# Kernel optimization log

Measured on AMD Instinct MI355X. Metric: run time of the kernel, lower is better.

The kernel has to match this reference:

```python
import jax, jax.numpy as jnp
import numpy as np

N = 100000       # nodes
E = 1600000      # undirected edges (one direction stored)
D = 64           # feature_dim


def _linear_params(key, fan_in, fan_out):
    kw, kb = jax.random.split(key)
    s = 1.0 / np.sqrt(fan_in)
    W = jax.random.uniform(kw, (fan_in, fan_out), jnp.float32, -s, s)
    b = jax.random.uniform(kb, (fan_out,), jnp.float32, -s, s)
    return W, b


def setup_inputs() -> dict:
    key = jax.random.key(0)
    ks = jax.random.split(key, 8)
    node_features = jax.random.normal(ks[0], (N, D), jnp.float32)
    node_operations = jax.random.normal(ks[1], (N, 4), jnp.float32)

    # Unique undirected edges, no self-loops -> torch's set() dedup of
    # {outgoing} U {incoming} neighbors equals counting each stored edge once
    # in both directions.
    rng = np.random.default_rng(0)
    src = rng.integers(0, N, size=4 * E)
    dst = rng.integers(0, N, size=4 * E)
    lo, hi = np.minimum(src, dst), np.maximum(src, dst)
    keep = lo != hi
    pairs = np.unique(np.stack([lo[keep], hi[keep]], axis=1), axis=0)
    assert pairs.shape[0] >= E
    perm = rng.permutation(pairs.shape[0])[:E]
    edge_index = jnp.asarray(pairs[perm].T, dtype=jnp.int32)  # [2, E]

    # node_generator: Linear(2D,128)-ReLU-Linear(128,64)-ReLU-Linear(64,D+3)
    W1, b1 = _linear_params(ks[2], 2 * D, 128)
    W2, b2 = _linear_params(ks[3], 128, 64)
    W3, b3 = _linear_params(ks[4], 64, D + 3)
    # insertion_predictor: Linear(D,32)-ReLU-Linear(32,1)-Sigmoid
    P1, pb1 = _linear_params(ks[5], D, 32)
    P2, pb2 = _linear_params(ks[6], 32, 1)

    return {
        'node_features': node_features,
        'node_operations': node_operations,
        'edge_index': edge_index,
        'W1': W1, 'b1': b1, 'W2': W2, 'b2': b2, 'W3': W3, 'b3': b3,
        'P1': P1, 'pb1': pb1, 'P2': P2, 'pb2': pb2,
    }


def reference(node_features, node_operations, edge_index,
              W1, b1, W2, b2, W3, b3, P1, pb1, P2, pb2):
    n = node_features.shape[0]
    src, dst = edge_index[0], edge_index[1]

    # candidate mask: softmax over op logits, class 0 = insert, threshold 0.5
    insert_probs = jax.nn.softmax(node_operations, axis=-1)[:, 0]
    ones = jnp.ones(src.shape[0], node_features.dtype)
    deg = (jax.ops.segment_sum(ones, src, num_segments=n)
           + jax.ops.segment_sum(ones, dst, num_segments=n))
    # torch loop skips candidates with no neighbors
    mask = (insert_probs > 0.5) & (deg > 0)
    maskf = mask.astype(node_features.dtype)

    # batched neighbor mean (undirected: both edge directions)
    nsum = (jax.ops.segment_sum(node_features[dst], src, num_segments=n)
            + jax.ops.segment_sum(node_features[src], dst, num_segments=n))
    nmean = nsum / jnp.maximum(deg, 1.0)[:, None]

    ctx = jnp.concatenate([node_features, nmean], axis=-1)  # [N, 2D]
    h = jax.nn.relu(ctx @ W1 + b1)
    h = jax.nn.relu(h @ W2 + b2)
    gen = h @ W3 + b3                         # [N, D+3]
    pos = gen[:, :3]                          # [N, 3]
    feats = gen[:, 3:]                        # [N, D]
    p = jax.nn.relu(feats @ P1 + pb1)
    prob = jax.nn.sigmoid(p @ P2 + pb2)       # [N, 1]

    # pack: [positions | features | probability], zeroed for non-candidates
    out = jnp.concatenate([pos, feats, prob], axis=-1) * maskf[:, None]
    return out
```

## Files before the change

### kernel.cpp

```cpp
#include <hip/hip_runtime.h>
#include <hip/hip_bf16.h>
#include <hip/hip_fp16.h>
#include <math.h>

typedef unsigned int u32;
typedef unsigned short u16;
typedef unsigned long long u64;

#define O_W1 0
#define O_b1 16384
#define O_W2 16512
#define O_b2 24704
#define O_W3 24768
#define O_b3 29056
#define O_P1 29123
#define O_pb1 31171
#define O_P2 31203
#define O_pb2 31235
#define W_TOTAL 31236

#define NPB 16
#define LDW 17

__device__ __forceinline__ float ldf(const void* p, long i, int dt) {
  if (dt == 1) { u32 v = ((const u16*)p)[i]; return __uint_as_float(v << 16); }
  if (dt == 2) { __half h = ((const __half*)p)[i]; return __half2float(h); }
  return ((const float*)p)[i];
}
__device__ __forceinline__ int ldei(const int* p, long i, int is64) {
  return is64 ? p[2 * i] : p[i];
}
__device__ __forceinline__ int bit_test(const u64* bits, int i) {
  return (int)((bits[i >> 6] >> (i & 63)) & 1ull);
}

extern "C" __global__ void kall_detect(const u32* __restrict__ feat,
                                       const u32* __restrict__ w1,
                                       const u32* __restrict__ ops,
                                       const u32* __restrict__ ei,
                                       int* __restrict__ hdr)
{
  int lane = threadIdx.x;
  int mode = blockIdx.x;
  if (mode == 3) {
    unsigned long long m0 = __ballot(ei[lane] == 0u);
    unsigned long long m1 = __ballot(ei[64 + lane] == 0u);
    if (lane == 0) hdr[2] = (__popcll(m0) + __popcll(m1) >= 32) ? 1 : 0;
    return;
  }
  const u32* p = (mode == 0) ? feat : (mode == 1) ? w1 : ops;
  int slot = (mode == 0) ? 0 : (mode == 1) ? 1 : 3;
  u32 w0 = p[lane];
  u32 w1v = p[64 + lane];
  u16 h[4] = { (u16)(w0 & 0xffff), (u16)(w0 >> 16),
               (u16)(w1v & 0xffff), (u16)(w1v >> 16) };
  int cb = 0;
#pragma unroll
  for (int t = 0; t < 4; ++t) {
    int e8 = (h[t] >> 7) & 0xff;
    cb += (e8 >= 110 && e8 <= 140) ? 1 : 0;
  }
  int ch = 0;
#pragma unroll
  for (int t = 0; t < 4; t += 2) {
    int e5 = (h[t] >> 10) & 0x1f;
    ch += (e5 >= 5 && e5 <= 18) ? 1 : 0;
  }
  __shared__ int sb[64], sh[64];
  sb[lane] = cb; sh[lane] = ch;
  __syncthreads();
  if (lane == 0) {
    int CB = 0, CH = 0;
    for (int t = 0; t < 64; ++t) { CB += sb[t]; CH += sh[t]; }
    int dt;
    if (CB >= 200) dt = 1;
    else if (CH >= 100) dt = 2;
    else dt = 0;
    hdr[slot] = dt;
  }
}

extern "C" __global__ void __launch_bounds__(256)
kw_conv(const void* __restrict__ W1, const void* __restrict__ b1,
        const void* __restrict__ W2, const void* __restrict__ b2,
        const void* __restrict__ W3, const void* __restrict__ b3,
        const void* __restrict__ P1, const void* __restrict__ pb1,
        const void* __restrict__ P2, const void* __restrict__ pb2,
        const int* __restrict__ hdr, float* __restrict__ wf)
{
  int i = blockIdx.x * 256 + threadIdx.x;
  if (i >= W_TOTAL) return;
  const void* s; int o;
  if      (i < O_b1)  { s = W1;  o = i; }
  else if (i < O_W2)  { s = b1;  o = i - O_b1; }
  else if (i < O_b2)  { s = W2;  o = i - O_W2; }
  else if (i < O_W3)  { s = b2;  o = i - O_b2; }
  else if (i < O_b3)  { s = W3;  o = i - O_W3; }
  else if (i < O_P1)  { s = b3;  o = i - O_b3; }
  else if (i < O_pb1) { s = P1;  o = i - O_P1; }
  else if (i < O_P2)  { s = pb1; o = i - O_pb1; }
  else if (i < O_pb2) { s = P2;  o = i - O_P2; }
  else                { s = pb2; o = i - O_pb2; }
  wf[i] = ldf(s, o, hdr[1]);
}

extern "C" __global__ void __launch_bounds__(256)
k2a_cand(const void* __restrict__ opsv, const int* __restrict__ hdr,
         u64* __restrict__ bits, int* __restrict__ cnt,
         int* __restrict__ fillcnt, int N)
{
  int i = blockIdx.x * 256 + threadIdx.x;
  if (i >= N) return;
  cnt[i] = 0;
  fillcnt[i] = 0;
  int dt = hdr[3];
  float x0 = ldf(opsv, (long)i * 4 + 0, dt);
  float x1 = ldf(opsv, (long)i * 4 + 1, dt);
  float x2 = ldf(opsv, (long)i * 4 + 2, dt);
  float x3 = ldf(opsv, (long)i * 4 + 3, dt);
  float m = fmaxf(fmaxf(x0, x1), fmaxf(x2, x3));
  double e0 = exp((double)(x0 - m));
  double e1 = exp((double)(x1 - m));
  double e2 = exp((double)(x2 - m));
  double e3 = exp((double)(x3 - m));
  double p0 = e0 / (((e0 + e1) + e2) + e3);
  u64 msk = __ballot(p0 > 0.5);
  if ((threadIdx.x & 63) == 0) bits[i >> 6] = msk;
}

extern "C" __global__ void __launch_bounds__(256)
k1a_cnt(const int* __restrict__ ei, const u64* __restrict__ bits,
        int* __restrict__ cnt, int E, const int* __restrict__ hdr)
{
  int e = blockIdx.x * 256 + threadIdx.x;
  if (e >= E) return;
  int is64 = hdr[2];
  int s = ldei(ei, e, is64);
  int d = ldei(ei, (long)E + e, is64);
  if (bit_test(bits, s)) atomicAdd(cnt + s, 1);
  if (bit_test(bits, d)) atomicAdd(cnt + d, 1);
}

extern "C" __global__ void __launch_bounds__(256)
k2b_alloc(const u64* __restrict__ bits, const int* __restrict__ cnt,
          int* __restrict__ hdr, int* __restrict__ nodeoff,
          int* __restrict__ nlist, int N)
{
  int i = blockIdx.x * 256 + threadIdx.x;
  if (i >= N) return;
  int c = (bit_test(bits, i) && cnt[i] > 0) ? cnt[i] : 0;
  if (c > 0) {
    int pos = atomicAdd(hdr + 4, 1);
    nlist[pos] = i;
    nodeoff[i] = atomicAdd(hdr + 5, c);
  } else {
    nodeoff[i] = -1;
  }
}

extern "C" __global__ void __launch_bounds__(256)
k1_fill(const int* __restrict__ ei, const u64* __restrict__ bits,
        const int* __restrict__ nodeoff,
        int* __restrict__ fillcnt, int* __restrict__ adj, int E,
        const int* __restrict__ hdr)
{
  int e = blockIdx.x * 256 + threadIdx.x;
  if (e >= E) return;
  int is64 = hdr[2];
  int s = ldei(ei, e, is64);
  int d = ldei(ei, (long)E + e, is64);
  if (bit_test(bits, s)) {
    int os = nodeoff[s];
    if (os >= 0) { int p = atomicAdd(fillcnt + s, 1); adj[os + p] = d; }
  }
  if (bit_test(bits, d)) {
    int od = nodeoff[d];
    if (od >= 0) { int p = atomicAdd(fillcnt + d, 1); adj[od + p] = s; }
  }
}

extern "C" __global__ void __launch_bounds__(256)
k3b_mlp(const void* __restrict__ featv, const int* __restrict__ nlist,
        const int* __restrict__ cnt, const int* __restrict__ nodeoff,
        const int* __restrict__ adj,
        const float* __restrict__ wf, const int* __restrict__ hdr,
        float* __restrict__ out)
{
  __shared__ float A[128 * LDW];
  __shared__ float B[128 * LDW];
  __shared__ float WS[4096];
  __shared__ int sNode[NPB];
  __shared__ int sDeg[NPB];
  __shared__ int sOff[NPB];
  const int tid = threadIdx.x;
  const int nmask = hdr[4];
  const int base = blockIdx.x * NPB;
  if (nmask == 0 || base >= nmask) return;
  const int dt = hdr[0];
  const int nl = tid & 15;
  const int jg = tid >> 4;
  const int lane = tid & 63;
  const int q = __builtin_amdgcn_readfirstlane(tid >> 6);

  if (tid < NPB) {
    int idx = base + tid;
    int node = nlist[(idx < nmask) ? idx : (nmask - 1)];
    sNode[tid] = node;
    sDeg[tid] = cnt[node];
    sOff[tid] = nodeoff[node];
  }
  __syncthreads();

#pragma unroll
  for (int i = 0; i < 4; ++i) {
    int g = i * 256 + tid;
    int f = g & 63;
    int n = g >> 6;
    int node = sNode[n];
    A[f * LDW + n] = ldf(featv, (long)node * 64 + f, dt);
  }

  if (dt == 0) {
    const float4* f4 = (const float4*)featv;
    const int g = lane >> 4;
    const int fq = lane & 15;
#pragma unroll
    for (int t = 0; t < 4; ++t) {
      const int n = q * 4 + t;
      const int off = sOff[n];
      const int dg = sDeg[n];
      float4 acc = make_float4(0.f, 0.f, 0.f, 0.f);
      int j = g;
      for (; j + 4 < dg; j += 8) {
        int n0 = adj[off + j];
        int n1 = adj[off + j + 4];
        float4 v0 = f4[(long)n0 * 16 + fq];
        float4 v1 = f4[(long)n1 * 16 + fq];
        acc.x += v0.x + v1.x; acc.y += v0.y + v1.y;
        acc.z += v0.z + v1.z; acc.w += v0.w + v1.w;
      }
      if (j < dg) {
        int n0 = adj[off + j];
        float4 v0 = f4[(long)n0 * 16 + fq];
        acc.x += v0.x; acc.y += v0.y; acc.z += v0.z; acc.w += v0.w;
      }
      acc.x += __shfl_xor(acc.x, 16); acc.y += __shfl_xor(acc.y, 16);
      acc.z += __shfl_xor(acc.z, 16); acc.w += __shfl_xor(acc.w, 16);
      acc.x += __shfl_xor(acc.x, 32); acc.y += __shfl_xor(acc.y, 32);
      acc.z += __shfl_xor(acc.z, 32); acc.w += __shfl_xor(acc.w, 32);
      if (g == 0) {
        float inv = 1.f / (float)dg;
        A[(64 + fq * 4 + 0) * LDW + n] = acc.x * inv;
        A[(64 + fq * 4 + 1) * LDW + n] = acc.y * inv;
        A[(64 + fq * 4 + 2) * LDW + n] = acc.z * inv;
        A[(64 + fq * 4 + 3) * LDW + n] = acc.w * inv;
      }
    }
  } else {
#pragma unroll
    for (int t = 0; t < 4; ++t) {
      const int n = q * 4 + t;
      const int off = sOff[n];
      const int dg = sDeg[n];
      float acc = 0.f;
      int j = 0;
      for (; j + 4 <= dg; j += 4) {
        int n0 = adj[off + j + 0];
        int n1 = adj[off + j + 1];
        int n2 = adj[off + j + 2];
        int n3 = adj[off + j + 3];
        float v0 = ldf(featv, (long)n0 * 64 + lane, dt);
        float v1 = ldf(featv, (long)n1 * 64 + lane, dt);
        float v2 = ldf(featv, (long)n2 * 64 + lane, dt);
        float v3 = ldf(featv, (long)n3 * 64 + lane, dt);
        acc += ((v0 + v1) + (v2 + v3));
      }
      for (; j < dg; ++j)
        acc += ldf(featv, (long)adj[off + j] * 64 + lane, dt);
      A[(64 + lane) * LDW + n] = acc / (float)dg;
    }
  }

  {
    const int j0 = jg * 8;
    float a0 = wf[O_b1 + j0 + 0], a1 = wf[O_b1 + j0 + 1];
    float a2 = wf[O_b1 + j0 + 2], a3 = wf[O_b1 + j0 + 3];
    float a4 = wf[O_b1 + j0 + 4], a5 = wf[O_b1 + j0 + 5];
    float a6 = wf[O_b1 + j0 + 6], a7 = wf[O_b1 + j0 + 7];
    for (int c = 0; c < 4; ++c) {
      __syncthreads();
      {
        const float4* s4 = (const float4*)(wf + O_W1 + c * 4096);
        float4* d4 = (float4*)WS;
#pragma unroll
        for (int i = 0; i < 4; ++i) d4[tid + 256 * i] = s4[tid + 256 * i];
      }
      __syncthreads();
#pragma unroll 4
      for (int k = 0; k < 32; ++k) {
        float x = A[(c * 32 + k) * LDW + nl];
        const float* w = WS + k * 128 + j0;
        float4 w0 = *(const float4*)(w);
        float4 w1 = *(const float4*)(w + 4);
        a0 = fmaf(x, w0.x, a0);
        a1 = fmaf(x, w0.y, a1);
        a2 = fmaf(x, w0.z, a2);
        a3 = fmaf(x, w0.w, a3);
        a4 = fmaf(x, w1.x, a4);
        a5 = fmaf(x, w1.y, a5);
        a6 = fmaf(x, w1.z, a6);
        a7 = fmaf(x, w1.w, a7);
      }
    }
    B[(j0 + 0) * LDW + nl] = fmaxf(a0, 0.f);
    B[(j0 + 1) * LDW + nl] = fmaxf(a1, 0.f);
    B[(j0 + 2) * LDW + nl] = fmaxf(a2, 0.f);
    B[(j0 + 3) * LDW + nl] = fmaxf(a3, 0.f);
    B[(j0 + 4) * LDW + nl] = fmaxf(a4, 0.f);
    B[(j0 + 5) * LDW + nl] = fmaxf(a5, 0.f);
    B[(j0 + 6) * LDW + nl] = fmaxf(a6, 0.f);
    B[(j0 + 7) * LDW + nl] = fmaxf(a7, 0.f);
  }

  {
    const int j0 = jg * 4;
    float a0 = wf[O_b2 + j0 + 0], a1 = wf[O_b2 + j0 + 1];
    float a2 = wf[O_b2 + j0 + 2], a3 = wf[O_b2 + j0 + 3];
    for (int c = 0; c < 2; ++c) {
      __syncthreads();
      {
        const float4* s4 = (const float4*)(wf + O_W2 + c * 4096);
        float4* d4 = (float4*)WS;
#pragma unroll
        for (int i = 0; i < 4; ++i) d4[tid + 256 * i] = s4[tid + 256 * i];
      }
      __syncthreads();
#pragma unroll 4
      for (int k = 0; k < 64; ++k) {
        float x = B[(c * 64 + k) * LDW + nl];
        float4 w = *(const float4*)(WS + k * 64 + j0);
        a0 = fmaf(x, w.x, a0);
        a1 = fmaf(x, w.y, a1);
        a2 = fmaf(x, w.z, a2);
        a3 = fmaf(x, w.w, a3);
      }
    }
    A[(j0 + 0) * LDW + nl] = fmaxf(a0, 0.f);
    A[(j0 + 1) * LDW + nl] = fmaxf(a1, 0.f);
    A[(j0 + 2) * LDW + nl] = fmaxf(a2, 0.f);
    A[(j0 + 3) * LDW + nl] = fmaxf(a3, 0.f);
  }

  {
    const int jq = jg;
    const bool has5 = (jq < 3);
    float a0 = 0.f, a1 = 0.f, a2 = 0.f, a3 = 0.f, a4 = 0.f;
    for (int c = 0; c < 2; ++c) {
      __syncthreads();
      {
        const float4* s4 = (const float4*)(wf + O_W3 + c * 2144);
        float4* d4 = (float4*)WS;
        for (int i = tid; i < 536; i += 256) d4[i] = s4[i];
      }
      __syncthreads();
#pragma unroll 4
      for (int k = 0; k < 32; ++k) {
        float x = A[(c * 32 + k) * LDW + nl];
        const float* w = WS + k * 67 + jq;
        float w4 = has5 ? w[64] : 0.f;
        a0 = fmaf(x, w[0],  a0);
        a1 = fmaf(x, w[16], a1);
        a2 = fmaf(x, w[32], a2);
        a3 = fmaf(x, w[48], a3);
        a4 = fmaf(x, w4,    a4);
      }
    }
    B[(jq +  0) * LDW + nl] = wf[O_b3 + jq]      + a0;
    B[(jq + 16) * LDW + nl] = wf[O_b3 + jq + 16] + a1;
    B[(jq + 32) * LDW + nl] = wf[O_b3 + jq + 32] + a2;
    B[(jq + 48) * LDW + nl] = wf[O_b3 + jq + 48] + a3;
    if (has5)
      B[(jq + 64) * LDW + nl] = wf[O_b3 + jq + 64] + a4;
  }

  {
    const int jq = jg;
    float a0 = wf[O_pb1 + jq], a1 = wf[O_pb1 + jq + 16];
    __syncthreads();
    for (int i = tid; i < 2048; i += 256) WS[i] = wf[O_P1 + i];
    __syncthreads();
#pragma unroll 4
    for (int k = 0; k < 64; ++k) {
      float x = B[(3 + k) * LDW + nl];
      a0 = fmaf(x, WS[k * 32 + jq],      a0);
      a1 = fmaf(x, WS[k * 32 + jq + 16], a1);
    }
    A[(jq +  0) * LDW + nl] = fmaxf(a0, 0.f);
    A[(jq + 16) * LDW + nl] = fmaxf(a1, 0.f);
  }
  __syncthreads();

  if (tid < 64) {
    const int part = tid >> 4;
    float p = 0.f;
#pragma unroll
    for (int kk = 0; kk < 8; ++kk) {
      int k = part * 8 + kk;
      p = fmaf(A[k * LDW + nl], wf[O_P2 + k], p);
    }
    p += __shfl_xor(p, 16);
    p += __shfl_xor(p, 32);
    if (part == 0) {
      float z = wf[O_pb2] + p;
      B[67 * LDW + nl] = 1.0f / (1.0f + expf(-z));
    }
  }
  __syncthreads();

  for (int g = tid; g < NPB * 68; g += 256) {
    int n = g / 68;
    int c = g - n * 68;
    if (base + n < nmask) {
      int node = sNode[n];
      out[(long)node * 68 + c] = B[c * LDW + n];
    }
  }
}

extern "C" void kernel_launch(void* const* d_in, const int* in_sizes, int n_in,
                              void* d_out, int out_size, void* d_ws, size_t ws_size,
                              hipStream_t stream) {
  int iF = 0, iO = 1, iE = 2;
  int iW1 = 3, ib1 = 4, iW2 = 5, ib2 = 6, iW3 = 7, ib3 = 8;
  int iP1 = 9, ipb1 = 10, iP2 = 11, ipb2 = 12;
  {
    int bigs[4]; int nb = 0;
    for (int i = 0; i < n_in && nb < 4; ++i)
      if (in_sizes[i] > 100000) bigs[nb++] = i;
    if (nb == 3) {
      int a = bigs[0], b = bigs[1], c = bigs[2];
      int mx = a, mn = a;
      if (in_sizes[b] > in_sizes[mx]) mx = b;
      if (in_sizes[c] > in_sizes[mx]) mx = c;
      if (in_sizes[b] < in_sizes[mn]) mn = b;
      if (in_sizes[c] < in_sizes[mn]) mn = c;
      iF = mx; iO = mn; iE = a + b + c - mx - mn;
      int t32[2]; int n32 = 0;
      int jW1=-1, jb1=-1, jW2=-1, jb2=-1, jW3=-1, jb3=-1, jP1=-1, jpb2=-1;
      for (int i = 0; i < n_in; ++i) {
        if (i == iF || i == iO || i == iE) continue;
        switch (in_sizes[i]) {
          case 16384: jW1 = i; break;
          case 128:   jb1 = i; break;
          case 8192:  jW2 = i; break;
          case 64:    jb2 = i; break;
          case 4288:  jW3 = i; break;
          case 67:    jb3 = i; break;
          case 2048:  jP1 = i; break;
          case 1:     jpb2 = i; break;
          case 32:    if (n32 < 2) t32[n32++] = i; break;
          default: break;
        }
      }
      if (jW1 >= 0 && jb1 >= 0 && jW2 >= 0 && jb2 >= 0 && jW3 >= 0 &&
          jb3 >= 0 && jP1 >= 0 && jpb2 >= 0 && n32 == 2) {
        iW1 = jW1; ib1 = jb1; iW2 = jW2; ib2 = jb2; iW3 = jW3; ib3 = jb3;
        iP1 = jP1; ipb2 = jpb2;
        if (t32[1] == t32[0] + 1) { ipb1 = t32[0]; iP2 = t32[1]; }
        else                      { iP2 = t32[0]; ipb1 = t32[1]; }
      }
    }
  }
  int N = (out_size % 68 == 0) ? (out_size / 68) : (in_sizes[iF] / 64);
  const int E = in_sizes[iE] / 2;
  const void* feat = d_in[iF];
  const void* ops  = d_in[iO];
  const int* ei    = (const int*)d_in[iE];

  char* ws = (char*)d_ws;
  int* hdr = (int*)ws;
  size_t off = 256;
  float* wf = (float*)(ws + off);
  off += ((size_t)W_TOTAL * 4 + 255) & ~(size_t)255;
  u64* bits = (u64*)(ws + off);
  off += (((size_t)(N + 63) / 64) * 8 + 255) & ~(size_t)255;
  int* cnt = (int*)(ws + off);
  off += ((size_t)N * 4 + 255) & ~(size_t)255;
  int* nodeoff = (int*)(ws + off);
  off += ((size_t)N * 4 + 255) & ~(size_t)255;
  int* fillcnt = (int*)(ws + off);
  off += ((size_t)N * 4 + 255) & ~(size_t)255;
  int* nlist = (int*)(ws + off);
  off += ((size_t)N * 4 + 255) & ~(size_t)255;
  int* adj = (int*)(ws + off);

  hipMemsetAsync(hdr, 0, 256, stream);
  hipMemsetAsync(d_out, 0, (size_t)out_size * 4, stream);

  kall_detect<<<4, 64, 0, stream>>>((const u32*)feat, (const u32*)d_in[iW1],
                                    (const u32*)ops, (const u32*)ei, hdr);

  kw_conv<<<(W_TOTAL + 255) / 256, 256, 0, stream>>>(
      d_in[iW1], d_in[ib1], d_in[iW2], d_in[ib2], d_in[iW3], d_in[ib3],
      d_in[iP1], d_in[ipb1], d_in[iP2], d_in[ipb2], hdr, wf);
  k2a_cand<<<(N + 255) / 256, 256, 0, stream>>>(ops, hdr, bits, cnt, fillcnt, N);
  k1a_cnt<<<(E + 255) / 256, 256, 0, stream>>>(ei, bits, cnt, E, hdr);
  k2b_alloc<<<(N + 255) / 256, 256, 0, stream>>>(bits, cnt, hdr, nodeoff, nlist, N);
  k1_fill<<<(E + 255) / 256, 256, 0, stream>>>(ei, bits, nodeoff, fillcnt, adj, E, hdr);
  k3b_mlp<<<(N + NPB - 1) / NPB, 256, 0, stream>>>(feat, nlist, cnt, nodeoff,
                                                   adj, wf, hdr,
                                                   (float*)d_out);
}
```

Before: 241.2 us.

## Fuse prep kernels, vectorize edge passes, and batch allocation atomics per wavefront

Replaces the two memsets by zeroing inside kernels: the header reset moves into the detect kernel and the output rows are zeroed in a merged weight-conversion/candidate kernel. The edge count and fill kernels now handle four edges per thread with int4 loads. The fill kernel writes through a cursor array initialised to each node's start offset, so the separate nodeoff lookup is gone. Allocation uses a wavefront prefix scan with one pair of atomics per wave instead of per node. Together these cut launch overhead and atomic traffic, at the cost of more code paths and possible load imbalance per thread.

New measurement: 241.8 us. No clear change (+0.2%).

```diff
diff --git a/kernel.cpp b/kernel.cpp
--- a/kernel.cpp
+++ b/kernel.cpp
@@ -18,6 +18,7 @@
 #define O_P2 31203
 #define O_pb2 31235
 #define W_TOTAL 31236
+#define KWB ((W_TOTAL + 255) / 256)
 
 #define NPB 16
 #define LDW 17
@@ -43,6 +44,7 @@
   int lane = threadIdx.x;
   int mode = blockIdx.x;
   if (mode == 3) {
+    if (lane == 0) { hdr[4] = 0; hdr[5] = 0; }
     unsigned long long m0 = __ballot(ei[lane] == 0u);
     unsigned long long m1 = __ballot(ei[64 + lane] == 0u);
     if (lane == 0) hdr[2] = (__popcll(m0) + __popcll(m1) >= 32) ? 1 : 0;
@@ -81,38 +83,43 @@
 }
 
 extern "C" __global__ void __launch_bounds__(256)
-kw_conv(const void* __restrict__ W1, const void* __restrict__ b1,
-        const void* __restrict__ W2, const void* __restrict__ b2,
-        const void* __restrict__ W3, const void* __restrict__ b3,
-        const void* __restrict__ P1, const void* __restrict__ pb1,
-        const void* __restrict__ P2, const void* __restrict__ pb2,
-        const int* __restrict__ hdr, float* __restrict__ wf)
+k_prep(const void* __restrict__ W1, const void* __restrict__ b1,
+       const void* __restrict__ W2, const void* __restrict__ b2,
+       const void* __restrict__ W3, const void* __restrict__ b3,
+       const void* __restrict__ P1, const void* __restrict__ pb1,
+       const void* __restrict__ P2, const void* __restrict__ pb2,
+       const void* __restrict__ opsv, const int* __restrict__ hdr,
+       float* __restrict__ wf, u64* __restrict__ bits,
+       int* __restrict__ cnt, float* __restrict__ out, int N)
 {
-  int i = blockIdx.x * 256 + threadIdx.x;
-  if (i >= W_TOTAL) return;
-  const void* s; int o;
-  if      (i < O_b1)  { s = W1;  o = i; }
-  else if (i < O_W2)  { s = b1;  o = i - O_b1; }
-  else if (i < O_b2)  { s = W2;  o = i - O_W2; }
-  else if (i < O_W3)  { s = b2;  o = i - O_b2; }
-  else if (i < O_b3)  { s = W3;  o = i - O_W3; }
-  else if (i < O_P1)  { s = b3;  o = i - O_b3; }
-  else if (i < O_pb1) { s = P1;  o = i - O_P1; }
-  else if (i < O_P2)  { s = pb1; o = i - O_pb1; }
-  else if (i < O_pb2) { s = P2;  o = i - O_P2; }
-  else                { s = pb2; o = i - O_pb2; }
-  wf[i] = ldf(s, o, hdr[1]);
-}
-
-extern "C" __global__ void __launch_bounds__(256)
-k2a_cand(const void* __restrict__ opsv, const int* __restrict__ hdr,
-         u64* __restrict__ bits, int* __restrict__ cnt,
-         int* __restrict__ fillcnt, int N)
-{
-  int i = blockIdx.x * 256 + threadIdx.x;
+  const int b = blockIdx.x;
+  const int tid = threadIdx.x;
+  if (b < KWB) {
+    int i = b * 256 + tid;
+    if (i >= W_TOTAL) return;
+    const void* s; int o;
+    if      (i < O_b1)  { s = W1;  o = i; }
+    else if (i < O_W2)  { s = b1;  o = i - O_b1; }
+    else if (i < O_b2)  { s = W2;  o = i - O_W2; }
+    else if (i < O_W3)  { s = b2;  o = i - O_b2; }
+    else if (i < O_b3)  { s = W3;  o = i - O_W3; }
+    else if (i < O_P1)  { s = b3;  o = i - O_b3; }
+    else if (i < O_pb1) { s = P1;  o = i - O_P1; }
+    else if (i < O_P2)  { s = pb1; o = i - O_pb1; }
+    else if (i < O_pb2) { s = P2;  o = i - O_P2; }
+    else                { s = pb2; o = i - O_pb2; }
+    wf[i] = ldf(s, o, hdr[1]);
+    return;
+  }
+  int i = (b - KWB) * 256 + tid;
   if (i >= N) return;
   cnt[i] = 0;
-  fillcnt[i] = 0;
+  {
+    float4 z = make_float4(0.f, 0.f, 0.f, 0.f);
+    float4* orow = (float4*)(out + (long)i * 68);
+#pragma unroll
+    for (int t = 0; t < 17; ++t) orow[t] = z;
+  }
   int dt = hdr[3];
   float x0 = ldf(opsv, (long)i * 4 + 0, dt);
   float x1 = ldf(opsv, (long)i * 4 + 1, dt);
@@ -125,57 +132,105 @@
   double e3 = exp((double)(x3 - m));
   double p0 = e0 / (((e0 + e1) + e2) + e3);
   u64 msk = __ballot(p0 > 0.5);
-  if ((threadIdx.x & 63) == 0) bits[i >> 6] = msk;
+  if ((tid & 63) == 0) bits[i >> 6] = msk;
 }
 
 extern "C" __global__ void __launch_bounds__(256)
 k1a_cnt(const int* __restrict__ ei, const u64* __restrict__ bits,
         int* __restrict__ cnt, int E, const int* __restrict__ hdr)
 {
-  int e = blockIdx.x * 256 + threadIdx.x;
-  if (e >= E) return;
+  int t = blockIdx.x * 256 + threadIdx.x;
+  int e0 = t * 4;
+  if (e0 >= E) return;
   int is64 = hdr[2];
-  int s = ldei(ei, e, is64);
-  int d = ldei(ei, (long)E + e, is64);
-  if (bit_test(bits, s)) atomicAdd(cnt + s, 1);
-  if (bit_test(bits, d)) atomicAdd(cnt + d, 1);
+  if (!is64 && (E & 3) == 0 && e0 + 4 <= E) {
+    int4 sv = *(const int4*)(ei + e0);
+    int4 dv = *(const int4*)(ei + (long)E + e0);
+    if (bit_test(bits, sv.x)) atomicAdd(cnt + sv.x, 1);
+    if (bit_test(bits, sv.y)) atomicAdd(cnt + sv.y, 1);
+    if (bit_test(bits, sv.z)) atomicAdd(cnt + sv.z, 1);
+    if (bit_test(bits, sv.w)) atomicAdd(cnt + sv.w, 1);
+    if (bit_test(bits, dv.x)) atomicAdd(cnt + dv.x, 1);
+    if (bit_test(bits, dv.y)) atomicAdd(cnt + dv.y, 1);
+    if (bit_test(bits, dv.z)) atomicAdd(cnt + dv.z, 1);
+    if (bit_test(bits, dv.w)) atomicAdd(cnt + dv.w, 1);
+  } else {
+    int ee = (e0 + 4 < E) ? e0 + 4 : E;
+    for (int e = e0; e < ee; ++e) {
+      int s = ldei(ei, e, is64);
+      int d = ldei(ei, (long)E + e, is64);
+      if (bit_test(bits, s)) atomicAdd(cnt + s, 1);
+      if (bit_test(bits, d)) atomicAdd(cnt + d, 1);
+    }
+  }
 }
 
 extern "C" __global__ void __launch_bounds__(256)
 k2b_alloc(const u64* __restrict__ bits, const int* __restrict__ cnt,
           int* __restrict__ hdr, int* __restrict__ nodeoff,
-          int* __restrict__ nlist, int N)
+          int* __restrict__ fillcnt, int* __restrict__ nlist, int N)
 {
   int i = blockIdx.x * 256 + threadIdx.x;
-  if (i >= N) return;
-  int c = (bit_test(bits, i) && cnt[i] > 0) ? cnt[i] : 0;
+  int lane = threadIdx.x & 63;
+  int c = 0;
+  if (i < N && bit_test(bits, i)) { int cc = cnt[i]; if (cc > 0) c = cc; }
+  u64 act = __ballot(c > 0);
+  if (act == 0) { if (i < N) nodeoff[i] = -1; return; }
+  int cs = c;
+#pragma unroll
+  for (int d2 = 1; d2 < 64; d2 <<= 1) {
+    int tt = __shfl_up(cs, d2);
+    if (lane >= d2) cs += tt;
+  }
+  int excl = cs - c;
+  int ctot = __shfl(cs, 63);
+  int npos = __popcll(act);
+  int rank = __popcll(act & ((lane == 0) ? 0ull : (~0ull >> (64 - lane))));
+  int pb = 0, ob = 0;
+  if (lane == 0) {
+    pb = atomicAdd(hdr + 4, npos);
+    ob = atomicAdd(hdr + 5, ctot);
+  }
+  pb = __shfl(pb, 0);
+  ob = __shfl(ob, 0);
   if (c > 0) {
-    int pos = atomicAdd(hdr + 4, 1);
-    nlist[pos] = i;
-    nodeoff[i] = atomicAdd(hdr + 5, c);
-  } else {
+    nlist[pb + rank] = i;
+    int start = ob + excl;
+    nodeoff[i] = start;
+    fillcnt[i] = start;
+  } else if (i < N) {
     nodeoff[i] = -1;
   }
 }
 
 extern "C" __global__ void __launch_bounds__(256)
 k1_fill(const int* __restrict__ ei, const u64* __restrict__ bits,
-        const int* __restrict__ nodeoff,
-        int* __restrict__ fillcnt, int* __restrict__ adj, int E,
+        int* __restrict__ cur, int* __restrict__ adj, int E,
         const int* __restrict__ hdr)
 {
-  int e = blockIdx.x * 256 + threadIdx.x;
-  if (e >= E) return;
+  int t = blockIdx.x * 256 + threadIdx.x;
+  int e0 = t * 4;
+  if (e0 >= E) return;
   int is64 = hdr[2];
-  int s = ldei(ei, e, is64);
-  int d = ldei(ei, (long)E + e, is64);
-  if (bit_test(bits, s)) {
-    int os = nodeoff[s];
-    if (os >= 0) { int p = atomicAdd(fillcnt + s, 1); adj[os + p] = d; }
-  }
-  if (bit_test(bits, d)) {
-    int od = nodeoff[d];
-    if (od >= 0) { int p = atomicAdd(fillcnt + d, 1); adj[od + p] = s; }
+  if (!is64 && (E & 3) == 0 && e0 + 4 <= E) {
+    int4 sv = *(const int4*)(ei + e0);
+    int4 dv = *(const int4*)(ei + (long)E + e0);
+    if (bit_test(bits, sv.x)) { int p = atomicAdd(cur + sv.x, 1); adj[p] = dv.x; }
+    if (bit_test(bits, dv.x)) { int p = atomicAdd(cur + dv.x, 1); adj[p] = sv.x; }
+    if (bit_test(bits, sv.y)) { int p = atomicAdd(cur + sv.y, 1); adj[p] = dv.y; }
+    if (bit_test(bits, dv.y)) { int p = atomicAdd(cur + dv.y, 1); adj[p] = sv.y; }
+    if (bit_test(bits, sv.z)) { int p = atomicAdd(cur + sv.z, 1); adj[p] = dv.z; }
+    if (bit_test(bits, dv.z)) { int p = atomicAdd(cur + dv.z, 1); adj[p] = sv.z; }
+    if (bit_test(bits, sv.w)) { int p = atomicAdd(cur + sv.w, 1); adj[p] = dv.w; }
+    if (bit_test(bits, dv.w)) { int p = atomicAdd(cur + dv.w, 1); adj[p] = sv.w; }
+  } else {
+    int ee = (e0 + 4 < E) ? e0 + 4 : E;
+    for (int e = e0; e < ee; ++e) {
+      int s = ldei(ei, e, is64);
+      int d = ldei(ei, (long)E + e, is64);
+      if (bit_test(bits, s)) { int p = atomicAdd(cur + s, 1); adj[p] = d; }
+      if (bit_test(bits, d)) { int p = atomicAdd(cur + d, 1); adj[p] = s; }
+    }
   }
 }
 
@@ -494,19 +549,21 @@
   off += ((size_t)N * 4 + 255) & ~(size_t)255;
   int* adj = (int*)(ws + off);
 
-  hipMemsetAsync(hdr, 0, 256, stream);
-  hipMemsetAsync(d_out, 0, (size_t)out_size * 4, stream);
+  const int NB = (N + 255) / 256;
 
   kall_detect<<<4, 64, 0, stream>>>((const u32*)feat, (const u32*)d_in[iW1],
                                     (const u32*)ops, (const u32*)ei, hdr);
 
-  kw_conv<<<(W_TOTAL + 255) / 256, 256, 0, stream>>>(
+  k_prep<<<KWB + NB, 256, 0, stream>>>(
       d_in[iW1], d_in[ib1], d_in[iW2], d_in[ib2], d_in[iW3], d_in[ib3],
-      d_in[iP1], d_in[ipb1], d_in[iP2], d_in[ipb2], hdr, wf);
-  k2a_cand<<<(N + 255) / 256, 256, 0, stream>>>(ops, hdr, bits, cnt, fillcnt, N);
-  k1a_cnt<<<(E + 255) / 256, 256, 0, stream>>>(ei, bits, cnt, E, hdr);
-  k2b_alloc<<<(N + 255) / 256, 256, 0, stream>>>(bits, cnt, hdr, nodeoff, nlist, N);
-  k1_fill<<<(E + 255) / 256, 256, 0, stream>>>(ei, bits, nodeoff, fillcnt, adj, E, hdr);
+      d_in[iP1], d_in[ipb1], d_in[iP2], d_in[ipb2],
+      ops, hdr, wf, bits, cnt, (float*)d_out, N);
+
+  int eThreads = (E + 3) / 4;
+  k1a_cnt<<<(eThreads + 255) / 256, 256, 0, stream>>>(ei, bits, cnt, E, hdr);
+  k2b_alloc<<<NB, 256, 0, stream>>>(bits, cnt, hdr, nodeoff, fillcnt, nlist, N);
+  k1_fill<<<(eThreads + 255) / 256, 256, 0, stream>>>(ei, bits, fillcnt, adj,
+                                                      E, hdr);
   k3b_mlp<<<(N + NPB - 1) / NPB, 256, 0, stream>>>(feat, nlist, cnt, nodeoff,
                                                    adj, wf, hdr,
                                                    (float*)d_out);
```
